# Performance work log

Measured on AMD Instinct MI355X. Metric: run time of the kernel, lower is better.

The kernel has to match this reference:

```python
import jax, jax.numpy as jnp
import numpy as np

N, D, d = 4_000_000, 3, 2

def setup_inputs() -> dict:
    key = jax.random.key(0)
    k1, k2, k3 = jax.random.split(key, 3)
    points = jax.random.normal(k1, (N, D), dtype=jnp.float32)
    reconstructed_points = jax.random.normal(k2, (N, D), dtype=jnp.float32)
    orthonormal_frame = jax.random.normal(k3, (N, D, d), dtype=jnp.float32)
    return {"points": points, "reconstructed_points": reconstructed_points,
            "orthonormal_frame": orthonormal_frame}

def reference(points, reconstructed_points, orthonormal_frame):
    # r: [N, D] residual
    r = reconstructed_points - points
    # project r onto the tangent frame: y = H @ (H^T r), H: [N, D, d]
    coeffs = jnp.einsum('nij,ni->nj', orthonormal_frame, r)   # [N, d]
    y = jnp.einsum('nij,nj->ni', orthonormal_frame, coeffs)   # [N, D]
    # mean squared norm of the normal component
    diff = r - y
    return jnp.mean(jnp.sum(diff * diff, axis=1))
```

## Files before the change

### kernel.cpp

```cpp
#include <hip/hip_runtime.h>


#define THREADS 256
#define BLOCKS  2048
#define NWAVES  (THREADS / 64)

__global__ __launch_bounds__(THREADS) void ncrl_partial(
    const float* __restrict__ pts,
    const float* __restrict__ rec,
    const float* __restrict__ frame,
    float* __restrict__ partial,
    int nGroups)
{
    const float4* __restrict__ P4 = reinterpret_cast<const float4*>(pts);
    const float4* __restrict__ R4 = reinterpret_cast<const float4*>(rec);
    const float4* __restrict__ F4 = reinterpret_cast<const float4*>(frame);

    float acc = 0.0f;
    const int stride = gridDim.x * blockDim.x;
    for (int g = blockIdx.x * blockDim.x + threadIdx.x; g < nGroups; g += stride) {
        float4 a0 = P4[3 * g + 0], a1 = P4[3 * g + 1], a2 = P4[3 * g + 2];
        float4 b0 = R4[3 * g + 0], b1 = R4[3 * g + 1], b2 = R4[3 * g + 2];
        float4 h0 = F4[6 * g + 0], h1 = F4[6 * g + 1], h2 = F4[6 * g + 2];
        float4 h3 = F4[6 * g + 3], h4 = F4[6 * g + 4], h5 = F4[6 * g + 5];

        const float pa[12] = {a0.x, a0.y, a0.z, a0.w, a1.x, a1.y,
                              a1.z, a1.w, a2.x, a2.y, a2.z, a2.w};
        const float pb[12] = {b0.x, b0.y, b0.z, b0.w, b1.x, b1.y,
                              b1.z, b1.w, b2.x, b2.y, b2.z, b2.w};
        const float ph[24] = {h0.x, h0.y, h0.z, h0.w, h1.x, h1.y, h1.z, h1.w,
                              h2.x, h2.y, h2.z, h2.w, h3.x, h3.y, h3.z, h3.w,
                              h4.x, h4.y, h4.z, h4.w, h5.x, h5.y, h5.z, h5.w};

#pragma unroll
        for (int k = 0; k < 4; ++k) {
            const float r0 = pb[3 * k + 0] - pa[3 * k + 0];
            const float r1 = pb[3 * k + 1] - pa[3 * k + 1];
            const float r2 = pb[3 * k + 2] - pa[3 * k + 2];
            const float H00 = ph[6 * k + 0], H01 = ph[6 * k + 1];
            const float H10 = ph[6 * k + 2], H11 = ph[6 * k + 3];
            const float H20 = ph[6 * k + 4], H21 = ph[6 * k + 5];
            const float c0 = H00 * r0 + H10 * r1 + H20 * r2;
            const float c1 = H01 * r0 + H11 * r1 + H21 * r2;
            const float d0 = r0 - (H00 * c0 + H01 * c1);
            const float d1 = r1 - (H10 * c0 + H11 * c1);
            const float d2 = r2 - (H20 * c0 + H21 * c1);
            acc += d0 * d0 + d1 * d1 + d2 * d2;
        }
    }

#pragma unroll
    for (int off = 32; off > 0; off >>= 1)
        acc += __shfl_down(acc, off, 64);

    __shared__ float wsum[NWAVES];
    const int lane = threadIdx.x & 63;
    const int wv   = threadIdx.x >> 6;
    if (lane == 0) wsum[wv] = acc;
    __syncthreads();
    if (threadIdx.x == 0) {
        float s = 0.0f;
#pragma unroll
        for (int w = 0; w < NWAVES; ++w) s += wsum[w];
        partial[blockIdx.x] = s;
    }
}

__global__ __launch_bounds__(THREADS) void ncrl_finalize(
    const float* __restrict__ partial,
    const float* __restrict__ pts,
    const float* __restrict__ rec,
    const float* __restrict__ frame,
    float* __restrict__ out,
    int nPartial, int nTailStart, int nPoints)
{
    double acc = 0.0;
    for (int i = threadIdx.x; i < nPartial; i += THREADS)
        acc += (double)partial[i];

    if (threadIdx.x == 0) {
        for (int n = nTailStart; n < nPoints; ++n) {
            const float r0 = rec[3 * n + 0] - pts[3 * n + 0];
            const float r1 = rec[3 * n + 1] - pts[3 * n + 1];
            const float r2 = rec[3 * n + 2] - pts[3 * n + 2];
            const float H00 = frame[6 * n + 0], H01 = frame[6 * n + 1];
            const float H10 = frame[6 * n + 2], H11 = frame[6 * n + 3];
            const float H20 = frame[6 * n + 4], H21 = frame[6 * n + 5];
            const float c0 = H00 * r0 + H10 * r1 + H20 * r2;
            const float c1 = H01 * r0 + H11 * r1 + H21 * r2;
            const float d0 = r0 - (H00 * c0 + H01 * c1);
            const float d1 = r1 - (H10 * c0 + H11 * c1);
            const float d2 = r2 - (H20 * c0 + H21 * c1);
            acc += (double)(d0 * d0 + d1 * d1 + d2 * d2);
        }
    }

#pragma unroll
    for (int off = 32; off > 0; off >>= 1)
        acc += __shfl_down(acc, off, 64);

    __shared__ double wsum[NWAVES];
    const int lane = threadIdx.x & 63;
    const int wv   = threadIdx.x >> 6;
    if (lane == 0) wsum[wv] = acc;
    __syncthreads();
    if (threadIdx.x == 0) {
        double total = 0.0;
#pragma unroll
        for (int w = 0; w < NWAVES; ++w) total += wsum[w];
        out[0] = (float)(total / (double)nPoints);
    }
}

extern "C" void kernel_launch(void* const* d_in, const int* in_sizes, int n_in,
                              void* d_out, int out_size, void* d_ws, size_t ws_size,
                              hipStream_t stream) {
    const float* pts   = (const float*)d_in[0];
    const float* rec   = (const float*)d_in[1];
    const float* frame = (const float*)d_in[2];
    float* out = (float*)d_out;

    const int N       = in_sizes[0] / 3;
    const int nGroups = N / 4;
    const int tail    = nGroups * 4;

    float* partial = (float*)d_ws;

    ncrl_partial<<<BLOCKS, THREADS, 0, stream>>>(pts, rec, frame, partial, nGroups);
    ncrl_finalize<<<1, THREADS, 0, stream>>>(partial, pts, rec, frame, out,
                                             BLOCKS, tail, N);
}
```

Measured before the change: 208.5 us.

## Stage inputs through LDS with direct global-to-LDS loads per wave slice

Each wave now copies a 256-point slice of points, reconstructions and frames straight into its own LDS region using global_load_lds 16-byte transfers. Each lane then reads its point's values from LDS, so global accesses stay fully coalesced while the per-point layout is handled in shared memory. The grid shrinks from 2048 to 768 blocks, and each block uses 48 KB of LDS, which limits occupancy. There is no double buffering: every iteration waits for all loads to finish before computing, so memory latency is exposed unless other waves hide it.

```diff
diff --git a/kernel.cpp b/kernel.cpp
--- a/kernel.cpp
+++ b/kernel.cpp
@@ -1,50 +1,73 @@
 #include <hip/hip_runtime.h>
+#include <stdint.h>
 
 
 #define THREADS 256
-#define BLOCKS  2048
 #define NWAVES  (THREADS / 64)
+#define BLOCKS  768
+#define WAVE_LDS 12288
+
+__device__ __forceinline__ void gload_lds16(const void* g, void* l) {
+    __builtin_amdgcn_global_load_lds(
+        (const __attribute__((address_space(1))) unsigned int*)g,
+        (__attribute__((address_space(3))) unsigned int*)l, 16, 0, 0);
+}
 
 __global__ __launch_bounds__(THREADS) void ncrl_partial(
     const float* __restrict__ pts,
     const float* __restrict__ rec,
     const float* __restrict__ frame,
     float* __restrict__ partial,
-    int nGroups)
+    int nSlices)
 {
-    const float4* __restrict__ P4 = reinterpret_cast<const float4*>(pts);
-    const float4* __restrict__ R4 = reinterpret_cast<const float4*>(rec);
-    const float4* __restrict__ F4 = reinterpret_cast<const float4*>(frame);
+    __shared__ char stage[WAVE_LDS * NWAVES];
+    __shared__ float wsum[NWAVES];
+
+    const int lane = threadIdx.x & 63;
+    const int wv   = threadIdx.x >> 6;
+    char* wbase = stage + wv * WAVE_LDS;
+    const float* Lp = (const float*)(wbase);
+    const float* Lr = (const float*)(wbase + 3072);
+    const float* Lf = (const float*)(wbase + 6144);
+
+    const float4* P4 = (const float4*)pts;
+    const float4* R4 = (const float4*)rec;
+    const float4* F4 = (const float4*)frame;
+
+    const int gw0      = blockIdx.x * NWAVES + wv;
+    const int gwStride = gridDim.x * NWAVES;
 
     float acc = 0.0f;
-    const int stride = gridDim.x * blockDim.x;
-    for (int g = blockIdx.x * blockDim.x + threadIdx.x; g < nGroups; g += stride) {
-        float4 a0 = P4[3 * g + 0], a1 = P4[3 * g + 1], a2 = P4[3 * g + 2];
-        float4 b0 = R4[3 * g + 0], b1 = R4[3 * g + 1], b2 = R4[3 * g + 2];
-        float4 h0 = F4[6 * g + 0], h1 = F4[6 * g + 1], h2 = F4[6 * g + 2];
-        float4 h3 = F4[6 * g + 3], h4 = F4[6 * g + 4], h5 = F4[6 * g + 5];
+    for (int s = gw0; s < nSlices; s += gwStride) {
+        asm volatile("s_waitcnt lgkmcnt(0)" ::: "memory");
 
-        const float pa[12] = {a0.x, a0.y, a0.z, a0.w, a1.x, a1.y,
-                              a1.z, a1.w, a2.x, a2.y, a2.z, a2.w};
-        const float pb[12] = {b0.x, b0.y, b0.z, b0.w, b1.x, b1.y,
-                              b1.z, b1.w, b2.x, b2.y, b2.z, b2.w};
-        const float ph[24] = {h0.x, h0.y, h0.z, h0.w, h1.x, h1.y, h1.z, h1.w,
-                              h2.x, h2.y, h2.z, h2.w, h3.x, h3.y, h3.z, h3.w,
-                              h4.x, h4.y, h4.z, h4.w, h5.x, h5.y, h5.z, h5.w};
+        const float4* Pg = P4 + (size_t)s * 192 + lane;
+        const float4* Rg = R4 + (size_t)s * 192 + lane;
+        const float4* Fg = F4 + (size_t)s * 384 + lane;
+#pragma unroll
+        for (int i = 0; i < 3; ++i) gload_lds16(Pg + i * 64, wbase + i * 1024);
+#pragma unroll
+        for (int i = 0; i < 3; ++i) gload_lds16(Rg + i * 64, wbase + 3072 + i * 1024);
+#pragma unroll
+        for (int i = 0; i < 6; ++i) gload_lds16(Fg + i * 64, wbase + 6144 + i * 1024);
+
+        asm volatile("s_waitcnt vmcnt(0)" ::: "memory");
 
 #pragma unroll
         for (int k = 0; k < 4; ++k) {
-            const float r0 = pb[3 * k + 0] - pa[3 * k + 0];
-            const float r1 = pb[3 * k + 1] - pa[3 * k + 1];
-            const float r2 = pb[3 * k + 2] - pa[3 * k + 2];
-            const float H00 = ph[6 * k + 0], H01 = ph[6 * k + 1];
-            const float H10 = ph[6 * k + 2], H11 = ph[6 * k + 3];
-            const float H20 = ph[6 * k + 4], H21 = ph[6 * k + 5];
-            const float c0 = H00 * r0 + H10 * r1 + H20 * r2;
-            const float c1 = H01 * r0 + H11 * r1 + H21 * r2;
-            const float d0 = r0 - (H00 * c0 + H01 * c1);
-            const float d1 = r1 - (H10 * c0 + H11 * c1);
-            const float d2 = r2 - (H20 * c0 + H21 * c1);
+            const int p = k * 64 + lane;
+            const float a0 = Lp[3 * p], a1 = Lp[3 * p + 1], a2 = Lp[3 * p + 2];
+            const float b0 = Lr[3 * p], b1 = Lr[3 * p + 1], b2 = Lr[3 * p + 2];
+            const float2 h0 = *(const float2*)(Lf + 6 * p);
+            const float2 h1 = *(const float2*)(Lf + 6 * p + 2);
+            const float2 h2 = *(const float2*)(Lf + 6 * p + 4);
+
+            const float r0 = b0 - a0, r1 = b1 - a1, r2 = b2 - a2;
+            const float c0 = h0.x * r0 + h1.x * r1 + h2.x * r2;
+            const float c1 = h0.y * r0 + h1.y * r1 + h2.y * r2;
+            const float d0 = r0 - (h0.x * c0 + h0.y * c1);
+            const float d1 = r1 - (h1.x * c0 + h1.y * c1);
+            const float d2 = r2 - (h2.x * c0 + h2.y * c1);
             acc += d0 * d0 + d1 * d1 + d2 * d2;
         }
     }
@@ -53,16 +76,13 @@
     for (int off = 32; off > 0; off >>= 1)
         acc += __shfl_down(acc, off, 64);
 
-    __shared__ float wsum[NWAVES];
-    const int lane = threadIdx.x & 63;
-    const int wv   = threadIdx.x >> 6;
     if (lane == 0) wsum[wv] = acc;
     __syncthreads();
     if (threadIdx.x == 0) {
-        float s = 0.0f;
+        float ssum = 0.0f;
 #pragma unroll
-        for (int w = 0; w < NWAVES; ++w) s += wsum[w];
-        partial[blockIdx.x] = s;
+        for (int w = 0; w < NWAVES; ++w) ssum += wsum[w];
+        partial[blockIdx.x] = ssum;
     }
 }
 
@@ -99,15 +119,15 @@
     for (int off = 32; off > 0; off >>= 1)
         acc += __shfl_down(acc, off, 64);
 
-    __shared__ double wsum[NWAVES];
+    __shared__ double dsum[NWAVES];
     const int lane = threadIdx.x & 63;
     const int wv   = threadIdx.x >> 6;
-    if (lane == 0) wsum[wv] = acc;
+    if (lane == 0) dsum[wv] = acc;
     __syncthreads();
     if (threadIdx.x == 0) {
         double total = 0.0;
 #pragma unroll
-        for (int w = 0; w < NWAVES; ++w) total += wsum[w];
+        for (int w = 0; w < NWAVES; ++w) total += dsum[w];
         out[0] = (float)(total / (double)nPoints);
     }
 }
@@ -121,12 +141,12 @@
     float* out = (float*)d_out;
 
     const int N       = in_sizes[0] / 3;
-    const int nGroups = N / 4;
-    const int tail    = nGroups * 4;
+    const int nSlices = N / 256;
+    const int tail    = nSlices * 256;
 
     float* partial = (float*)d_ws;
 
-    ncrl_partial<<<BLOCKS, THREADS, 0, stream>>>(pts, rec, frame, partial, nGroups);
+    ncrl_partial<<<BLOCKS, THREADS, 0, stream>>>(pts, rec, frame, partial, nSlices);
     ncrl_finalize<<<1, THREADS, 0, stream>>>(partial, pts, rec, frame, out,
                                              BLOCKS, tail, N);
 }
```

New measurement: 207.6 us. No clear change (-0.4%).
